# Kernel optimization log

Hardware: AMD Instinct MI355X
Metric: run time of the kernel (lower is better)

## Reference

```python
import jax, jax.numpy as jnp
import numpy as np

EPS = 1e-5

def conv2d(x, w, b=None, pad=0, groups=1):
    # x: NCHW, w: OIHW
    y = jax.lax.conv_general_dilated(
        x, w, window_strides=(1, 1), padding=[(pad, pad), (pad, pad)],
        dimension_numbers=('NCHW', 'OIHW', 'NCHW'), feature_group_count=groups)
    if b is not None:
        y = y + b[None, :, None, None]
    return y

def layernorm_c(x, w, b):
    # WithBias LayerNorm over channel dim of NCHW (matches to_3d -> LN(last dim=c) -> to_4d)
    mu = jnp.mean(x, axis=1, keepdims=True)
    var = jnp.mean((x - mu) ** 2, axis=1, keepdims=True)
    return (x - mu) / jnp.sqrt(var + EPS) * w[None, :, None, None] + b[None, :, None, None]

def setup_inputs() -> dict:
    key = jax.random.key(0)
    ks = iter(jax.random.split(key, 40))
    C, C8, Cc, Cs = 64, 8, 21, 2  # dim, dim//8, dim//compress_ratio, dim//squeeze_factor
    H = W = 64
    B = 4
    Hm = 128  # mlp hidden = dim * mlp_ratio
    s = 0.05
    def rn(shape):
        return jax.random.normal(next(ks), shape, dtype=jnp.float32) * s
    return {
        'x': jax.random.normal(next(ks), (B, C, H, W), dtype=jnp.float32),
        'ln_w': jnp.ones((C,), jnp.float32),
        'ln_b': jnp.zeros((C,), jnp.float32),
        'sab_q_w': rn((C8, C, 1, 1)), 'sab_q_b': rn((C8,)),
        'sab_k_w': rn((C8, C, 1, 1)), 'sab_k_b': rn((C8,)),
        'sab_v_w': rn((C, C, 1, 1)), 'sab_v_b': rn((C,)),
        'sab_qkdw_w': rn((C8, 1, 3, 3)), 'sab_qkdw_b': rn((C8,)),
        'sab_vdw_w': rn((C, 1, 3, 3)), 'sab_vdw_b': rn((C,)),
        'sab_proj_w': rn((C, C, 1, 1)), 'sab_proj_b': rn((C,)),
        'sab_gamma': jnp.zeros((1,), jnp.float32) + 0.1,
        'cab_w1': rn((Cc, C, 3, 3)), 'cab_b1': rn((Cc,)),
        'cab_w2': rn((C, Cc, 3, 3)), 'cab_b2': rn((C,)),
        'ca_w1': rn((Cs, C, 1, 1)), 'ca_b1': rn((Cs,)),
        'ca_w2': rn((C, Cs, 1, 1)), 'ca_b2': rn((C,)),
        'fc1_w': rn((Hm, C)), 'fc1_b': rn((Hm,)),
        'fc2_w': rn((C, Hm)), 'fc2_b': rn((C,)),
    }

def reference(x, ln_w, ln_b,
              sab_q_w, sab_q_b, sab_k_w, sab_k_b, sab_v_w, sab_v_b,
              sab_qkdw_w, sab_qkdw_b, sab_vdw_w, sab_vdw_b,
              sab_proj_w, sab_proj_b, sab_gamma,
              cab_w1, cab_b1, cab_w2, cab_b2,
              ca_w1, ca_b1, ca_w2, ca_b2,
              fc1_w, fc1_b, fc2_w, fc2_b):
    b, c, h, w = x.shape
    hw = h * w
    shortcut = x
    xn = layernorm_c(x, ln_w, ln_b)

    # --- SAB: full-pixel spatial self-attention ---
    C8 = sab_q_w.shape[0]
    q = conv2d(conv2d(xn, sab_q_w, sab_q_b), sab_qkdw_w, sab_qkdw_b, pad=1, groups=C8)
    k = conv2d(conv2d(xn, sab_k_w, sab_k_b), sab_qkdw_w, sab_qkdw_b, pad=1, groups=C8)
    v = conv2d(conv2d(xn, sab_v_w, sab_v_b), sab_vdw_w, sab_vdw_b, pad=1, groups=c)
    qf = q.reshape(b, C8, hw)          # (b, c8, n)
    kf = k.reshape(b, C8, hw)
    vf = v.reshape(b, c, hw)
    energy = jnp.einsum('bdi,bdj->bij', qf, kf)      # (b, hw, hw)
    attn = jax.nn.softmax(energy, axis=-1)
    out = jnp.einsum('bcj,bij->bci', vf, attn)        # (b, c, hw)
    out = out.reshape(b, c, h, w)
    out = conv2d(out, sab_proj_w, sab_proj_b)
    sa_feat = sab_gamma[0] * out + xn

    # --- CAB: conv compress/expand + RCAN channel attention ---
    y = conv2d(xn, cab_w1, cab_b1, pad=1)
    y = jax.nn.gelu(y, approximate=False)
    y = conv2d(y, cab_w2, cab_b2, pad=1)
    p = jnp.mean(y, axis=(2, 3), keepdims=True)       # adaptive avg pool to 1x1
    p = jax.nn.relu(conv2d(p, ca_w1, ca_b1))
    p = jax.nn.sigmoid(conv2d(p, ca_w2, ca_b2))
    ca_feat = y * p

    feat_sum = sa_feat + ca_feat + shortcut

    # --- MLP over channels (note: output is reshaped, NOT permuted back — faithful to source) ---
    fs1 = layernorm_c(feat_sum, ln_w, ln_b)
    t = fs1.transpose(0, 2, 3, 1).reshape(b, hw, c)   # (b, hw, c)
    t = jax.nn.gelu(t @ fc1_w.T + fc1_b, approximate=False)
    t = t @ fc2_w.T + fc2_b
    feat_sum2 = t.reshape(b, c, h, w)                 # raw view, matching torch .view(b,c,h,w)
    return feat_sum2 + feat_sum
```

## Files before the change

kernel.cpp:

```cpp
#include <hip/hip_runtime.h>
#include <math.h>

#define NB 4
#define NC 64
#define NC8 8
#define NCC 21
#define NHW 4096
#define NHM 128

typedef __attribute__((ext_vector_type(8))) short bf16x8;
typedef __attribute__((ext_vector_type(8))) unsigned short ushort8;
typedef __attribute__((ext_vector_type(4))) float f32x4;

__device__ __forceinline__ float gelu_exact(float x) {
    return 0.5f * x * (1.0f + erff(x * 0.70710678118654752f));
}

__device__ __forceinline__ unsigned short f2bf(float x) {
    union { float f; unsigned u; } u; u.f = x;
    unsigned r = u.u + 0x7fffu + ((u.u >> 16) & 1u);
    return (unsigned short)(r >> 16);
}

__device__ __forceinline__ float bf2f(unsigned short v) {
    union { unsigned u; float f; } t; t.u = (unsigned)v << 16; return t.f;
}

__global__ void k_wt(const float* __restrict__ qw, const float* __restrict__ kw,
                     const float* __restrict__ vw, const float* __restrict__ c1w,
                     const float* __restrict__ c2w, const float* __restrict__ pw,
                     const float* __restrict__ f1w, const float* __restrict__ f2w,
                     float* __restrict__ o, float* __restrict__ pool) {
    int idx = blockIdx.x * 256 + threadIdx.x;
    if (idx < 256) pool[idx] = 0.f;
    if (idx < 5120) {
        int ci = idx / 80, j = idx - ci * 80;
        float v = j < 8 ? qw[j * 64 + ci] : (j < 16 ? kw[(j - 8) * 64 + ci] : vw[(j - 16) * 64 + ci]);
        o[idx] = v;
    } else if (idx < 9216) {
        int r = idx - 5120; int co = r & 63, ci = r >> 6;
        o[idx] = pw[co * 64 + ci];
    } else if (idx < 17408) {
        int r = idx - 9216; int m = r & 127, c = r >> 7;
        o[idx] = f1w[m * 64 + c];
    } else if (idx < 25600) {
        int r = idx - 17408; int wo = r & 63, m = r >> 6;
        o[idx] = f2w[wo * 128 + m];
    } else if (idx < 44032) {
        int r = idx - 25600;
        int j = r & 7, l = (r >> 3) & 63, s = (r >> 9) % 18, f = r / 9216;
        int co = f * 16 + (l & 15);
        int k = s * 32 + (l >> 4) * 8 + j;
        int tap = k >> 6, ci = k & 63;
        float v = (co < 21) ? c1w[co * 576 + ci * 9 + tap] : 0.f;
        unsigned short hi = f2bf(v);
        unsigned short lo = f2bf(v - bf2f(hi));
        ((unsigned short*)(o + 25600))[r] = hi;
        ((unsigned short*)(o + 34816))[r] = lo;
    } else if (idx < 62464) {
        int r = idx - 44032;
        int j = r & 7, l = (r >> 3) & 63, s = (r >> 9) % 9, f = r / 4608;
        int co = f * 16 + (l & 15);
        int ci = (l >> 4) * 8 + j;
        float v = (ci < 21) ? c2w[co * 189 + ci * 9 + s] : 0.f;
        unsigned short hi = f2bf(v);
        unsigned short lo = f2bf(v - bf2f(hi));
        ((unsigned short*)(o + 44032))[r] = hi;
        ((unsigned short*)(o + 53248))[r] = lo;
    }
}

__global__ __launch_bounds__(256) void k_ln(const float* __restrict__ in, const float* __restrict__ w,
                                            const float* __restrict__ bb,
                                            unsigned short* __restrict__ out,
                                            unsigned short* __restrict__ outT) {
    __shared__ float r1[4][64], r2[4][64];
    int tid = threadIdx.x;
    int pl = tid & 63, cq = tid >> 6;
    int b = blockIdx.x >> 6;
    int pix = (blockIdx.x & 63) * 64 + pl;
    const float* p = in + (size_t)b * NC * NHW + pix;
    float v[16]; float s = 0.f, ss = 0.f;
    #pragma unroll
    for (int k = 0; k < 16; ++k) {
        float f = p[(size_t)(cq * 16 + k) * NHW];
        v[k] = f; s += f; ss += f * f;
    }
    r1[cq][pl] = s; r2[cq][pl] = ss;
    __syncthreads();
    float S  = r1[0][pl] + r1[1][pl] + r1[2][pl] + r1[3][pl];
    float SS = r2[0][pl] + r2[1][pl] + r2[2][pl] + r2[3][pl];
    float mean = S * (1.0f / 64);
    float rstd = rsqrtf(SS * (1.0f / 64) - mean * mean + 1e-5f);
    unsigned short* q = out + (size_t)b * NC * NHW + pix;
    ushort8 t0, t1;
    #pragma unroll
    for (int k = 0; k < 16; ++k) {
        int c = cq * 16 + k;
        unsigned short bv = f2bf((v[k] - mean) * rstd * w[c] + bb[c]);
        q[(size_t)c * NHW] = bv;
        if (k < 8) t0[k] = bv; else t1[k - 8] = bv;
    }
    unsigned short* tp = outT + ((size_t)b * NHW + pix) * 64 + cq * 16;
    *(ushort8*)tp = t0;
    *(ushort8*)(tp + 8) = t1;
}

__global__ __launch_bounds__(512) void k_qkv(const unsigned short* __restrict__ xn,
        const float* __restrict__ wt, const float* __restrict__ qb,
        const float* __restrict__ kb, const float* __restrict__ vb,
        unsigned short* __restrict__ q1, unsigned short* __restrict__ k1,
        unsigned short* __restrict__ v1) {
    __shared__ unsigned short Xs[64][64];
    __shared__ float Ws[64][80];
    int tid = threadIdx.x;
    int pix0 = blockIdx.x * 64, b = blockIdx.y;
    for (int i = tid; i < 1024; i += 512) {
        int c = i >> 4, q4 = i & 15;
        *(ushort4*)&Xs[c][q4 * 4] = *(const ushort4*)(xn + ((size_t)b * NC + c) * NHW + pix0 + q4 * 4);
    }
    for (int i = tid; i < 1280; i += 512)
        *(float4*)&((float*)Ws)[i * 4] = *(const float4*)&wt[i * 4];
    __syncthreads();
    int p2 = (tid & 31) * 2, g = tid >> 5;
    int co0 = g * 5;
    float a0[5], a1[5];
// ... 1 lines not shown
    for (int j = 0; j < 5; ++j) { a0[j] = 0.f; a1[j] = 0.f; }
    for (int ci = 0; ci < 64; ++ci) {
        ushort2 uv = *(const ushort2*)&Xs[ci][p2];
        float fx = bf2f(uv.x), fy = bf2f(uv.y);
        #pragma unroll
        for (int j = 0; j < 5; ++j) {
            float wv = Ws[ci][co0 + j];
            a0[j] = fmaf(fx, wv, a0[j]);
            a1[j] = fmaf(fy, wv, a1[j]);
        }
    }
    #pragma unroll
    for (int j = 0; j < 5; ++j) {
        int co = co0 + j;
        float bsv; unsigned short* dst;
        if (co < 8)       { bsv = qb[co];      dst = q1 + ((size_t)b * NC8 + co) * NHW + pix0 + p2; }
        else if (co < 16) { bsv = kb[co - 8];  dst = k1 + ((size_t)b * NC8 + co - 8) * NHW + pix0 + p2; }
        else              { bsv = vb[co - 16]; dst = v1 + ((size_t)b * NC + co - 16) * NHW + pix0 + p2; }
        ushort2 o = { f2bf(a0[j] + bsv), f2bf(a1[j] + bsv) };
        *(ushort2*)dst = o;
    }
}

__global__ void k_dw(const unsigned short* __restrict__ q1, const unsigned short* __restrict__ k1,
                     const unsigned short* __restrict__ v1,
                     const float* __restrict__ qkw, const float* __restrict__ qkb,
                     const float* __restrict__ vw, const float* __restrict__ vb,
                     unsigned short* __restrict__ qdb, unsigned short* __restrict__ kdb,
                     unsigned short* __restrict__ v8) {
    int pix = blockIdx.x * blockDim.x + threadIdx.x;
    int yv = blockIdx.y, b = blockIdx.z;
    int y = pix >> 6, x = pix & 63;
    if (yv < 16) {
        int c = yv & 7;
        const unsigned short* ip = (yv < 8 ? q1 : k1) + ((size_t)b * NC8 + c) * NHW;
        const float* wp = qkw + c * 9;
        float acc = qkb[c];
        #pragma unroll
        for (int dy = -1; dy <= 1; ++dy) {
            int yy = y + dy; if (yy < 0 || yy > 63) continue;
            #pragma unroll
            for (int dx = -1; dx <= 1; ++dx) {
                int xx = x + dx; if (xx < 0 || xx > 63) continue;
                acc += wp[(dy + 1) * 3 + (dx + 1)] * bf2f(ip[yy * 64 + xx]);
            }
        }
        (yv < 8 ? qdb : kdb)[((size_t)b * NHW + pix) * NC8 + c] = f2bf(acc);
    } else {
        int c = yv - 16;
        const unsigned short* ip = v1 + ((size_t)b * NC + c) * NHW;
        const float* wp = vw + c * 9;
        float acc = vb[c];
        #pragma unroll
        for (int dy = -1; dy <= 1; ++dy) {
            int yy = y + dy; if (yy < 0 || yy > 63) continue;
            #pragma unroll
            for (int dx = -1; dx <= 1; ++dx) {
                int xx = x + dx; if (xx < 0 || xx > 63) continue;
                acc += wp[(dy + 1) * 3 + (dx + 1)] * bf2f(ip[yy * 64 + xx]);
            }
        }
        v8[(((size_t)b * 512 + (pix >> 3)) * NC + c) * 8 + (pix & 7)] = f2bf(acc);
    }
}

__global__ __launch_bounds__(512) void k_cab1(const unsigned short* __restrict__ xnT,
        const unsigned short* __restrict__ Ah, const unsigned short* __restrict__ Al,
        const float* __restrict__ bias, unsigned short* __restrict__ y1T) {
    __shared__ float Rs[2048];
    int tid = threadIdx.x;
    int w = tid >> 6, lane = tid & 63;
    int il = lane & 15, g = lane >> 4;
    int frag = w & 3, kh = w >> 2;
    int y = blockIdx.x, b = blockIdx.y;
    int xloc = frag * 16 + il;
    f32x4 acc[2];
    acc[0] = (f32x4){0.f, 0.f, 0.f, 0.f};
    acc[1] = (f32x4){0.f, 0.f, 0.f, 0.f};
    #pragma unroll
    for (int si = 0; si < 9; ++si) {
        int s = kh * 9 + si;
        int tap = s >> 1;
        int ci0 = (s & 1) * 32;
        int dyv = tap / 3 - 1, dxv = tap - (tap / 3) * 3 - 1;
        int xx = xloc + dxv, yy = y + dyv;
        bf16x8 bv = (bf16x8)(short)0;
        if (((unsigned)xx < 64u) && ((unsigned)yy < 64u))
            bv = *(const bf16x8*)(xnT + ((size_t)b * NHW + yy * 64 + xx) * 64 + ci0 + g * 8);
        #pragma unroll
        for (int f = 0; f < 2; ++f) {
            bf16x8 ahv = *(const bf16x8*)(Ah + ((size_t)(f * 18 + s) * 64 + lane) * 8);
            bf16x8 alv = *(const bf16x8*)(Al + ((size_t)(f * 18 + s) * 64 + lane) * 8);
            acc[f] = __builtin_amdgcn_mfma_f32_16x16x32_bf16(ahv, bv, acc[f], 0, 0, 0);
            acc[f] = __builtin_amdgcn_mfma_f32_16x16x32_bf16(alv, bv, acc[f], 0, 0, 0);
        }
    }
    if (kh == 1) {
        #pragma unroll
        for (int f = 0; f < 2; ++f)
            #pragma unroll
            for (int e = 0; e < 4; ++e)
                Rs[((frag * 2 + f) * 4 + e) * 64 + lane] = acc[f][e];
    }
    __syncthreads();
    if (kh == 0) {
        #pragma unroll
        for (int f = 0; f < 2; ++f) {
            ushort4 pk;
            #pragma unroll
            for (int e = 0; e < 4; ++e) {
                float v = acc[f][e] + Rs[((frag * 2 + f) * 4 + e) * 64 + lane];
                int co = f * 16 + g * 4 + e;
                float r = 0.f;
                if (co < 21) r = gelu_exact(v + bias[co]);
                ((unsigned short*)&pk)[e] = f2bf(r);
            }
            *(ushort4*)(y1T + ((size_t)b * NHW + y * 64 + xloc) * 32 + f * 16 + g * 4) = pk;
        }
    }
}

__global__ __launch_bounds__(512) void k_cab2(const unsigned short* __restrict__ y1T,
        const unsigned short* __restrict__ Ah, const unsigned short* __restrict__ Al,
        const float* __restrict__ bias, unsigned short* __restrict__ ycT,
        float* __restrict__ pool) {
    __shared__ float Rs[4096];
    __shared__ float Ssum[4][64];
    int tid = threadIdx.x;
    int w = tid >> 6, lane = tid & 63;
    int il = lane & 15, g = lane >> 4;
    int frag = w & 3, kh = w >> 2;
    int y = blockIdx.x, b = blockIdx.y;
    int xloc = frag * 16 + il;
    f32x4 acc[4];
    #pragma unroll
    for (int f = 0; f < 4; ++f) acc[f] = (f32x4){0.f, 0.f, 0.f, 0.f};
    #pragma unroll
    for (int si = 0; si < 5; ++si) {
        if (!(kh == 1 && si == 4)) {
            int s = kh * 5 + si;
            int dyv = s / 3 - 1, dxv = s - (s / 3) * 3 - 1;
            int xx = xloc + dxv, yy = y + dyv;
            bf16x8 bv = (bf16x8)(short)0;
            if (((unsigned)xx < 64u) && ((unsigned)yy < 64u))
                bv = *(const bf16x8*)(y1T + ((size_t)b * NHW + yy * 64 + xx) * 32 + g * 8);
            #pragma unroll
            for (int f = 0; f < 4; ++f) {
                bf16x8 ahv = *(const bf16x8*)(Ah + ((size_t)(f * 9 + s) * 64 + lane) * 8);
                bf16x8 alv = *(const bf16x8*)(Al + ((size_t)(f * 9 + s) * 64 + lane) * 8);
                acc[f] = __builtin_amdgcn_mfma_f32_16x16x32_bf16(ahv, bv, acc[f], 0, 0, 0);
                acc[f] = __builtin_amdgcn_mfma_f32_16x16x32_bf16(alv, bv, acc[f], 0, 0, 0);
            }
        }
    }
    if (kh == 1) {
// ... 7 lines not shown
    if (kh == 0) {
        #pragma unroll
        for (int f = 0; f < 4; ++f) {
            ushort4 pk;
            #pragma unroll
            for (int e = 0; e < 4; ++e) {
                int co = f * 16 + g * 4 + e;
                float v = acc[f][e] + Rs[((frag * 4 + f) * 4 + e) * 64 + lane] + bias[co];
                ((unsigned short*)&pk)[e] = f2bf(v);
                float ps = v;
                ps += __shfl_xor(ps, 1, 64);
                ps += __shfl_xor(ps, 2, 64);
                ps += __shfl_xor(ps, 4, 64);
                ps += __shfl_xor(ps, 8, 64);
                if (il == 0) Ssum[frag][co] = ps;
            }
            *(ushort4*)(ycT + ((size_t)b * NHW + y * 64 + xloc) * 64 + f * 16 + g * 4) = pk;
        }
    }
    __syncthreads();
    if (tid < 64) {
        float t = Ssum[0][tid] + Ssum[1][tid] + Ssum[2][tid] + Ssum[3][tid];
        atomicAdd(&pool[b * NC + tid], t);
    }
}

__global__ __launch_bounds__(512) void k_flash(const unsigned short* __restrict__ qdb,
                                               const unsigned short* __restrict__ kdb,
                                               const unsigned short* __restrict__ v8,
                                               unsigned short* __restrict__ O) {
    __shared__ __align__(16) char smem[35840];
    int tid = threadIdx.x;
    int w = tid >> 6, lane = tid & 63;
    int g = lane >> 4, il = lane & 15;
    int i0 = blockIdx.x * 32, b = blockIdx.y;

    unsigned short (*P)[72] = (unsigned short (*)[72])(smem + w * 2304);

    bf16x8 qb0 = (bf16x8)(short)0, qb1 = (bf16x8)(short)0;
    if (g == 0) {
        qb0 = *(const bf16x8*)(qdb + (size_t)(b * NHW + i0 + il) * NC8);
        qb1 = *(const bf16x8*)(qdb + (size_t)(b * NHW + i0 + 16 + il) * NC8);
    }

    f32x4 acc0[4], acc1[4];
    #pragma unroll
    for (int ct = 0; ct < 4; ++ct) {
        acc0[ct] = (f32x4){0.f, 0.f, 0.f, 0.f};
        acc1[ct] = (f32x4){0.f, 0.f, 0.f, 0.f};
    }
    float La0 = 0.f, La1 = 0.f;

    bf16x8 kn[4];
    #pragma unroll
    for (int t = 0; t < 4; ++t) {
        kn[t] = (bf16x8)(short)0;
        if (g == 0) kn[t] = *(const bf16x8*)(kdb + (size_t)(b * NHW + w * 512 + 16 * t + il) * NC8);
    }

    for (int jt = 0; jt < 8; ++jt) {
        int j0 = w * 512 + jt * 64;
        int ch0 = b * 512 + (j0 >> 3);
        bf16x8 va[2][4];
        #pragma unroll
        for (int kc = 0; kc < 2; ++kc)
            #pragma unroll
            for (int ct = 0; ct < 4; ++ct)
                va[kc][ct] = *(const bf16x8*)(v8 +
                    ((size_t)(ch0 + kc * 4 + g) * NC + ct * 16 + il) * 8);
        bf16x8 ka[4];
        #pragma unroll
        for (int t = 0; t < 4; ++t) ka[t] = kn[t];
        if (jt < 7) {
            #pragma unroll
            for (int t = 0; t < 4; ++t) {
                kn[t] = (bf16x8)(short)0;
                if (g == 0) kn[t] = *(const bf16x8*)(kdb + (size_t)(b * NHW + j0 + 64 + 16 * t + il) * NC8);
            }
        }
        #pragma unroll
        for (int t = 0; t < 4; ++t) {
            f32x4 sv = __builtin_amdgcn_mfma_f32_16x16x32_bf16(ka[t], qb0, (f32x4){0.f, 0.f, 0.f, 0.f}, 0, 0, 0);
            float p0 = __expf(sv[0]), p1 = __expf(sv[1]);
            float p2 = __expf(sv[2]), p3 = __expf(sv[3]);
            La0 += (p0 + p1) + (p2 + p3);
            ushort4 pk;
            pk.x = f2bf(p0); pk.y = f2bf(p1); pk.z = f2bf(p2); pk.w = f2bf(p3);
            *(ushort4*)&P[il][16 * t + 4 * g] = pk;
        }
        #pragma unroll
        for (int kc = 0; kc < 2; ++kc) {
            bf16x8 pb = *(const bf16x8*)&P[il][kc * 32 + 8 * g];
            #pragma unroll
            for (int ct = 0; ct < 4; ++ct)
                acc0[ct] = __builtin_amdgcn_mfma_f32_16x16x32_bf16(va[kc][ct], pb, acc0[ct], 0, 0, 0);
        }
        #pragma unroll
        for (int t = 0; t < 4; ++t) {
            f32x4 sv = __builtin_amdgcn_mfma_f32_16x16x32_bf16(ka[t], qb1, (f32x4){0.f, 0.f, 0.f, 0.f}, 0, 0, 0);
            float p0 = __expf(sv[0]), p1 = __expf(sv[1]);
            float p2 = __expf(sv[2]), p3 = __expf(sv[3]);
            La1 += (p0 + p1) + (p2 + p3);
            ushort4 pk;
            pk.x = f2bf(p0); pk.y = f2bf(p1); pk.z = f2bf(p2); pk.w = f2bf(p3);
            *(ushort4*)&P[il][16 * t + 4 * g] = pk;
        }
        #pragma unroll
        for (int kc = 0; kc < 2; ++kc) {
            bf16x8 pb = *(const bf16x8*)&P[il][kc * 32 + 8 * g];
            #pragma unroll
            for (int ct = 0; ct < 4; ++ct)
                acc1[ct] = __builtin_amdgcn_mfma_f32_16x16x32_bf16(va[kc][ct], pb, acc1[ct], 0, 0, 0);
        }
    }
    La0 += __shfl_xor(La0, 16, 64); La0 += __shfl_xor(La0, 32, 64);
    La1 += __shfl_xor(La1, 16, 64); La1 += __shfl_xor(La1, 32, 64);

    __syncthreads();
    unsigned short* Ocm = (unsigned short*)smem;
    float* Lw = (float*)(smem + 34816);
    #pragma unroll
    for (int ct = 0; ct < 4; ++ct)
        #pragma unroll
        for (int e = 0; e < 4; ++e) {
            int c = ct * 16 + 4 * g + e;
            Ocm[(w * 2 + 0) * 1088 + c * 17 + il] = f2bf(acc0[ct][e]);
            Ocm[(w * 2 + 1) * 1088 + c * 17 + il] = f2bf(acc1[ct][e]);
        }
    if (lane < 16) {
        Lw[(w * 2 + 0) * 16 + il] = La0;
        Lw[(w * 2 + 1) * 16 + il] = La1;
    }
    __syncthreads();

    int st = tid >> 8, rem = tid & 255;
    int ic = rem & 15, ch = rem >> 4;
    float l = 0.f;
    #pragma unroll
    for (int w2 = 0; w2 < 8; ++w2) l += Lw[(w2 * 2 + st) * 16 + ic];
    float rl = 1.0f / l;
    #pragma unroll
    for (int cc = 0; cc < 4; ++cc) {
        int c = cc * 16 + ch;
        float o = 0.f;
        #pragma unroll
        for (int w2 = 0; w2 < 8; ++w2) o += bf2f(Ocm[(w2 * 2 + st) * 1088 + c * 17 + ic]);
        O[(size_t)(b * NC + c) * NHW + i0 + st * 16 + ic] = f2bf(o * rl);
    }
}

__global__ __launch_bounds__(512) void k_fsum2(const unsigned short* __restrict__ O,
        const float* __restrict__ pwt, const float* __restrict__ pb,
        const float* __restrict__ gamma, const unsigned short* __restrict__ xnT,
        const unsigned short* __restrict__ ycT, const float* __restrict__ pool,
        const float* __restrict__ cw1, const float* __restrict__ cb1,
        const float* __restrict__ cw2, const float* __restrict__ cb2,
        const float* __restrict__ x, const float* __restrict__ lnw,
        const float* __restrict__ lnb, unsigned short* __restrict__ fsum,
        unsigned short* __restrict__ fs1) {
    __shared__ unsigned short Os[64][64];
    __shared__ float Ws[64][64];
    __shared__ float Fs[64][66];
    __shared__ float mean_s[64], rstd_s[64];
    int tid = threadIdx.x;
    int pix0 = blockIdx.x * 64, b = blockIdx.y;
    for (int i = tid; i < 1024; i += 512) {
        int c = i >> 4, q4 = i & 15;
        *(ushort4*)&Os[c][q4 * 4] = *(const ushort4*)(O + ((size_t)b * NC + c) * NHW + pix0 + q4 * 4);
    }
    for (int i = tid; i < 1024; i += 512)
// ... 52 lines not shown
    }
    __syncthreads();
    if (tid < 64) {
        float s = 0.f, ss = 0.f;
        for (int c = 0; c < 64; ++c) { float v = Fs[c][tid]; s += v; ss += v * v; }
        float mean = s * (1.0f / 64);
        mean_s[tid] = mean;
        rstd_s[tid] = rsqrtf(ss * (1.0f / 64) - mean * mean + 1e-5f);
    }
    __syncthreads();
    float m0 = mean_s[p2], r0 = rstd_s[p2];
    float m1 = mean_s[p2 + 1], r1 = rstd_s[p2 + 1];
    #pragma unroll
    for (int j = 0; j < 4; ++j) {
        int c = co0 + j;
        size_t n = base + (size_t)c * NHW;
        float lw = lnw[c], lb = lnb[c];
        ushort2 o = { f2bf((f0[j] - m0) * r0 * lw + lb),
                      f2bf((f1[j] - m1) * r1 * lw + lb) };
        *(ushort2*)&fs1[n] = o;
    }
}

__global__ __launch_bounds__(512) void k_mlp1(const unsigned short* __restrict__ fs1,
        const float* __restrict__ wt, const float* __restrict__ bias,
        unsigned short* __restrict__ h) {
    __shared__ unsigned short Fs[64][64];
    __shared__ float Ws[64][128];
    int tid = threadIdx.x;
    int pix0 = blockIdx.x * 64, b = blockIdx.y;
    for (int i = tid; i < 1024; i += 512) {
        int c = i >> 4, q4 = i & 15;
        *(ushort4*)&Fs[c][q4 * 4] = *(const ushort4*)(fs1 + ((size_t)b * NC + c) * NHW + pix0 + q4 * 4);
    }
    for (int i = tid; i < 2048; i += 512)
        *(float4*)&((float*)Ws)[i * 4] = *(const float4*)&wt[i * 4];
    __syncthreads();
    int p2 = (tid & 31) * 2, g = tid >> 5;
    int m0 = g * 8;
    float a0[8], a1[8];
    #pragma unroll
    for (int j = 0; j < 8; ++j) { float bv = bias[m0 + j]; a0[j] = bv; a1[j] = bv; }
    for (int c = 0; c < 64; ++c) {
        ushort2 uv = *(const ushort2*)&Fs[c][p2];
        float vx = bf2f(uv.x), vy = bf2f(uv.y);
        float wv[8];
        *(float4*)&wv[0] = *(const float4*)&Ws[c][m0];
        *(float4*)&wv[4] = *(const float4*)&Ws[c][m0 + 4];
        #pragma unroll
        for (int j = 0; j < 8; ++j) {
            a0[j] = fmaf(vx, wv[j], a0[j]);
            a1[j] = fmaf(vy, wv[j], a1[j]);
        }
    }
    unsigned short* hp = h + (size_t)b * NHM * NHW + pix0 + p2;
    #pragma unroll
    for (int j = 0; j < 8; ++j) {
        ushort2 o = { f2bf(gelu_exact(a0[j])), f2bf(gelu_exact(a1[j])) };
        *(ushort2*)(hp + (size_t)(m0 + j) * NHW) = o;
    }
}

__global__ __launch_bounds__(512) void k_mlp2(const unsigned short* __restrict__ h,
        const float* __restrict__ wt, const float* __restrict__ bias,
        const unsigned short* __restrict__ fs, float* __restrict__ out) {
    __shared__ unsigned short Hs[128][64];
    __shared__ float Ws[128][64];
    int tid = threadIdx.x;
    int pix0 = blockIdx.x * 64, b = blockIdx.y;
    for (int i = tid; i < 2048; i += 512) {
        int m = i >> 4, q4 = i & 15;
        *(ushort4*)&Hs[m][q4 * 4] = *(const ushort4*)(h + ((size_t)b * NHM + m) * NHW + pix0 + q4 * 4);
    }
    for (int i = tid; i < 2048; i += 512)
        *(float4*)&((float*)Ws)[i * 4] = *(const float4*)&wt[i * 4];
    __syncthreads();
    int p2 = (tid & 31) * 2, g = tid >> 5;
    int wo0 = g * 4;
    float a0[4], a1[4];
    #pragma unroll
    for (int j = 0; j < 4; ++j) { float bv = bias[wo0 + j]; a0[j] = bv; a1[j] = bv; }
    for (int m = 0; m < 128; ++m) {
        ushort2 uv = *(const ushort2*)&Hs[m][p2];
        float vx = bf2f(uv.x), vy = bf2f(uv.y);
        float wv[4];
        *(float4*)wv = *(const float4*)&Ws[m][wo0];
        #pragma unroll
        for (int j = 0; j < 4; ++j) {
            a0[j] = fmaf(vx, wv[j], a0[j]);
            a1[j] = fmaf(vy, wv[j], a1[j]);
        }
    }
    size_t ob0 = ((size_t)b * NHW + pix0 + p2) * 64 + wo0;
    ushort4 r0 = *(const ushort4*)&fs[ob0];
    ushort4 r1 = *(const ushort4*)&fs[ob0 + 64];
    float4 w0, w1;
    w0.x = a0[0] + bf2f(r0.x); w0.y = a0[1] + bf2f(r0.y);
    w0.z = a0[2] + bf2f(r0.z); w0.w = a0[3] + bf2f(r0.w);
    w1.x = a1[0] + bf2f(r1.x); w1.y = a1[1] + bf2f(r1.y);
    w1.z = a1[2] + bf2f(r1.z); w1.w = a1[3] + bf2f(r1.w);
    *(float4*)&out[ob0] = w0;
    *(float4*)&out[ob0 + 64] = w1;
}

extern "C" void kernel_launch(void* const* d_in, const int* in_sizes, int n_in,
                              void* d_out, int out_size, void* d_ws, size_t ws_size,
                              hipStream_t stream) {
    const float* x        = (const float*)d_in[0];
    const float* ln_w     = (const float*)d_in[1];
// ... 22 lines not shown
    const float* fc1_w    = (const float*)d_in[24];
    const float* fc1_b    = (const float*)d_in[25];
    const float* fc2_w    = (const float*)d_in[26];
    const float* fc2_b    = (const float*)d_in[27];
    float* out = (float*)d_out;

    char* ws = (char*)d_ws;
    size_t off = 0;
    auto alloc = [&](size_t bytes) { void* p = ws + off; off += (bytes + 255) & ~(size_t)255; return p; };
    unsigned short* xn  = (unsigned short*)alloc((size_t)NB * NC * NHW * 2);
    unsigned short* xnT = (unsigned short*)alloc((size_t)NB * NHW * NC * 2);
    unsigned short* q1  = (unsigned short*)alloc((size_t)NB * NC8 * NHW * 2);
    unsigned short* k1  = (unsigned short*)alloc((size_t)NB * NC8 * NHW * 2);
    unsigned short* v1  = (unsigned short*)alloc((size_t)NB * NC * NHW * 2);
    unsigned short* qdb = (unsigned short*)alloc((size_t)NB * NHW * NC8 * 2);
    unsigned short* kdb = (unsigned short*)alloc((size_t)NB * NHW * NC8 * 2);
    unsigned short* vdb = (unsigned short*)alloc((size_t)NB * NC * NHW * 2);
    unsigned short* O   = (unsigned short*)alloc((size_t)NB * NC * NHW * 2);
    unsigned short* y1T = (unsigned short*)alloc((size_t)NB * NHW * 32 * 2);
    unsigned short* ycT = (unsigned short*)alloc((size_t)NB * NHW * NC * 2);
    float* pool  = (float*)alloc(256 * 4);
    unsigned short* fsum = (unsigned short*)alloc((size_t)NB * NC * NHW * 2);
    unsigned short* fs1  = (unsigned short*)alloc((size_t)NB * NC * NHW * 2);
    unsigned short* hbuf = (unsigned short*)alloc((size_t)NB * NHM * NHW * 2);
    float* wpack = (float*)alloc(62464 * 4);

    float* qkv_wt  = wpack;
    float* proj_wt = wpack + 5120;
    float* fc1_wt  = wpack + 9216;
    float* fc2_wt  = wpack + 17408;
    unsigned short* cab1Ah = (unsigned short*)(wpack + 25600);
    unsigned short* cab1Al = (unsigned short*)(wpack + 34816);
    unsigned short* cab2Ah = (unsigned short*)(wpack + 44032);
    unsigned short* cab2Al = (unsigned short*)(wpack + 53248);

    dim3 blk(256);
    dim3 blk5(512);

    k_wt<<<dim3(244), blk, 0, stream>>>(q_w, k_w, v_w, cab_w1, cab_w2, proj_w, fc1_w, fc2_w, wpack, pool);
    k_ln<<<dim3(256), blk, 0, stream>>>(x, ln_w, ln_b, xn, xnT);
    k_qkv<<<dim3(64, NB), blk5, 0, stream>>>(xn, qkv_wt, q_b, k_b, v_b, q1, k1, v1);
    k_dw<<<dim3(16, 80, NB), blk, 0, stream>>>(q1, k1, v1, qkdw_w, qkdw_b, vdw_w, vdw_b, qdb, kdb, vdb);
    k_cab1<<<dim3(64, NB), blk5, 0, stream>>>(xnT, cab1Ah, cab1Al, cab_b1, y1T);
    k_flash<<<dim3(128, NB), blk5, 0, stream>>>(qdb, kdb, vdb, O);
    k_cab2<<<dim3(64, NB), blk5, 0, stream>>>(y1T, cab2Ah, cab2Al, cab_b2, ycT, pool);
    k_fsum2<<<dim3(64, NB), blk5, 0, stream>>>(O, proj_wt, proj_b, gamma, xnT, ycT, pool,
                                               ca_w1, ca_b1, ca_w2, ca_b2, x, ln_w, ln_b,
                                               fsum, fs1);
    k_mlp1<<<dim3(64, NB), blk5, 0, stream>>>(fs1, fc1_wt, fc1_b, hbuf);
    k_mlp2<<<dim3(64, NB), blk5, 0, stream>>>(hbuf, fc2_wt, fc2_b, fsum, out);
}
```

Measured before the change: 206.8 us.

## Merge independent kernels into shared launches and fuse MLP stages in shared memory

```diff
diff --git a/kernel.cpp b/kernel.cpp
--- a/kernel.cpp
+++ b/kernel.cpp
@@ -26,60 +26,62 @@
     union { unsigned u; float f; } t; t.u = (unsigned)v << 16; return t.f;
 }
 
-__global__ void k_wt(const float* __restrict__ qw, const float* __restrict__ kw,
+__global__ __launch_bounds__(256) void k_prep(const float* __restrict__ qw, const float* __restrict__ kw,
                      const float* __restrict__ vw, const float* __restrict__ c1w,
                      const float* __restrict__ c2w, const float* __restrict__ pw,
                      const float* __restrict__ f1w, const float* __restrict__ f2w,
-                     float* __restrict__ o, float* __restrict__ pool) {
-    int idx = blockIdx.x * 256 + threadIdx.x;
-    if (idx < 256) pool[idx] = 0.f;
-    if (idx < 5120) {
-        int ci = idx / 80, j = idx - ci * 80;
-        float v = j < 8 ? qw[j * 64 + ci] : (j < 16 ? kw[(j - 8) * 64 + ci] : vw[(j - 16) * 64 + ci]);
-        o[idx] = v;
-    } else if (idx < 9216) {
-        int r = idx - 5120; int co = r & 63, ci = r >> 6;
-        o[idx] = pw[co * 64 + ci];
-    } else if (idx < 17408) {
-        int r = idx - 9216; int m = r & 127, c = r >> 7;
-        o[idx] = f1w[m * 64 + c];
-    } else if (idx < 25600) {
-        int r = idx - 17408; int wo = r & 63, m = r >> 6;
-        o[idx] = f2w[wo * 128 + m];
-    } else if (idx < 44032) {
-        int r = idx - 25600;
-        int j = r & 7, l = (r >> 3) & 63, s = (r >> 9) % 18, f = r / 9216;
-        int co = f * 16 + (l & 15);
-        int k = s * 32 + (l >> 4) * 8 + j;
-        int tap = k >> 6, ci = k & 63;
-        float v = (co < 21) ? c1w[co * 576 + ci * 9 + tap] : 0.f;
-        unsigned short hi = f2bf(v);
-        unsigned short lo = f2bf(v - bf2f(hi));
-        ((unsigned short*)(o + 25600))[r] = hi;
-        ((unsigned short*)(o + 34816))[r] = lo;
-    } else if (idx < 62464) {
-        int r = idx - 44032;
-        int j = r & 7, l = (r >> 3) & 63, s = (r >> 9) % 9, f = r / 4608;
-        int co = f * 16 + (l & 15);
-        int ci = (l >> 4) * 8 + j;
-        float v = (ci < 21) ? c2w[co * 189 + ci * 9 + s] : 0.f;
-        unsigned short hi = f2bf(v);
-        unsigned short lo = f2bf(v - bf2f(hi));
-        ((unsigned short*)(o + 44032))[r] = hi;
-        ((unsigned short*)(o + 53248))[r] = lo;
-    }
-}
-
-__global__ __launch_bounds__(256) void k_ln(const float* __restrict__ in, const float* __restrict__ w,
-                                            const float* __restrict__ bb,
-                                            unsigned short* __restrict__ out,
-                                            unsigned short* __restrict__ outT) {
+                     float* __restrict__ o, float* __restrict__ pool,
+                     const float* __restrict__ x, const float* __restrict__ lnw,
+                     const float* __restrict__ lnb,
+                     unsigned short* __restrict__ xn, unsigned short* __restrict__ xnT) {
+    int bid = blockIdx.x;
+    int tid = threadIdx.x;
+    if (bid < 244) {
+        int idx = bid * 256 + tid;
+        if (idx < 256) pool[idx] = 0.f;
+        if (idx < 5120) {
+            int ci = idx / 80, j = idx - ci * 80;
+            float v = j < 8 ? qw[j * 64 + ci] : (j < 16 ? kw[(j - 8) * 64 + ci] : vw[(j - 16) * 64 + ci]);
+            o[idx] = v;
+        } else if (idx < 9216) {
+            int r = idx - 5120; int co = r & 63, ci = r >> 6;
+            o[idx] = pw[co * 64 + ci];
+        } else if (idx < 17408) {
+            int r = idx - 9216; int m = r & 127, c = r >> 7;
+            o[idx] = f1w[m * 64 + c];
+        } else if (idx < 25600) {
+            int r = idx - 17408; int wo = r & 63, m = r >> 6;
+            o[idx] = f2w[wo * 128 + m];
+        } else if (idx < 44032) {
+            int r = idx - 25600;
+            int j = r & 7, l = (r >> 3) & 63, s = (r >> 9) % 18, f = r / 9216;
+            int co = f * 16 + (l & 15);
+            int k = s * 32 + (l >> 4) * 8 + j;
+            int tap = k >> 6, ci = k & 63;
+            float v = (co < 21) ? c1w[co * 576 + ci * 9 + tap] : 0.f;
+            unsigned short hi = f2bf(v);
+            unsigned short lo = f2bf(v - bf2f(hi));
+            ((unsigned short*)(o + 25600))[r] = hi;
+            ((unsigned short*)(o + 34816))[r] = lo;
+        } else if (idx < 62464) {
+            int r = idx - 44032;
+            int j = r & 7, l = (r >> 3) & 63, s = (r >> 9) % 9, f = r / 4608;
+            int co = f * 16 + (l & 15);
+            int ci = (l >> 4) * 8 + j;
+            float v = (ci < 21) ? c2w[co * 189 + ci * 9 + s] : 0.f;
+            unsigned short hi = f2bf(v);
+            unsigned short lo = f2bf(v - bf2f(hi));
+            ((unsigned short*)(o + 44032))[r] = hi;
+            ((unsigned short*)(o + 53248))[r] = lo;
+        }
+        return;
+    }
     __shared__ float r1[4][64], r2[4][64];
-    int tid = threadIdx.x;
+    int lb = bid - 244;
     int pl = tid & 63, cq = tid >> 6;
-    int b = blockIdx.x >> 6;
-    int pix = (blockIdx.x & 63) * 64 + pl;
-    const float* p = in + (size_t)b * NC * NHW + pix;
+    int b = lb >> 6;
+    int pix = (lb & 63) * 64 + pl;
+    const float* p = x + (size_t)b * NC * NHW + pix;
     float v[16]; float s = 0.f, ss = 0.f;
     #pragma unroll
     for (int k = 0; k < 16; ++k) {
@@ -92,16 +94,16 @@
     float SS = r2[0][pl] + r2[1][pl] + r2[2][pl] + r2[3][pl];
     float mean = S * (1.0f / 64);
     float rstd = rsqrtf(SS * (1.0f / 64) - mean * mean + 1e-5f);
-    unsigned short* q = out + (size_t)b * NC * NHW + pix;
+    unsigned short* q = xn + (size_t)b * NC * NHW + pix;
     ushort8 t0, t1;
     #pragma unroll
     for (int k = 0; k < 16; ++k) {
         int c = cq * 16 + k;
-        unsigned short bv = f2bf((v[k] - mean) * rstd * w[c] + bb[c]);
+        unsigned short bv = f2bf((v[k] - mean) * rstd * lnw[c] + lnb[c]);
         q[(size_t)c * NHW] = bv;
         if (k < 8) t0[k] = bv; else t1[k - 8] = bv;
     }
-    unsigned short* tp = outT + ((size_t)b * NHW + pix) * 64 + cq * 16;
+    unsigned short* tp = xnT + ((size_t)b * NHW + pix) * 64 + cq * 16;
     *(ushort8*)tp = t0;
     *(ushort8*)(tp + 8) = t1;
 }
@@ -149,57 +151,62 @@
     }
 }
 
-__global__ void k_dw(const unsigned short* __restrict__ q1, const unsigned short* __restrict__ k1,
-                     const unsigned short* __restrict__ v1,
-                     const float* __restrict__ qkw, const float* __restrict__ qkb,
-                     const float* __restrict__ vw, const float* __restrict__ vb,
-                     unsigned short* __restrict__ qdb, unsigned short* __restrict__ kdb,
-                     unsigned short* __restrict__ v8) {
-    int pix = blockIdx.x * blockDim.x + threadIdx.x;
-    int yv = blockIdx.y, b = blockIdx.z;
-    int y = pix >> 6, x = pix & 63;
-    if (yv < 16) {
-        int c = yv & 7;
-        const unsigned short* ip = (yv < 8 ? q1 : k1) + ((size_t)b * NC8 + c) * NHW;
-        const float* wp = qkw + c * 9;
-        float acc = qkb[c];
-        #pragma unroll
-        for (int dy = -1; dy <= 1; ++dy) {
-            int yy = y + dy; if (yy < 0 || yy > 63) continue;
-            #pragma unroll
-            for (int dx = -1; dx <= 1; ++dx) {
-                int xx = x + dx; if (xx < 0 || xx > 63) continue;
-                acc += wp[(dy + 1) * 3 + (dx + 1)] * bf2f(ip[yy * 64 + xx]);
-            }
-        }
-        (yv < 8 ? qdb : kdb)[((size_t)b * NHW + pix) * NC8 + c] = f2bf(acc);
-    } else {
-        int c = yv - 16;
-        const unsigned short* ip = v1 + ((size_t)b * NC + c) * NHW;
-        const float* wp = vw + c * 9;
-        float acc = vb[c];
-        #pragma unroll
-        for (int dy = -1; dy <= 1; ++dy) {
-            int yy = y + dy; if (yy < 0 || yy > 63) continue;
-            #pragma unroll
-            for (int dx = -1; dx <= 1; ++dx) {
-                int xx = x + dx; if (xx < 0 || xx > 63) continue;
-                acc += wp[(dy + 1) * 3 + (dx + 1)] * bf2f(ip[yy * 64 + xx]);
-            }
-        }
-        v8[(((size_t)b * 512 + (pix >> 3)) * NC + c) * 8 + (pix & 7)] = f2bf(acc);
-    }
-}
-
-__global__ __launch_bounds__(512) void k_cab1(const unsigned short* __restrict__ xnT,
+__global__ __launch_bounds__(512) void k_dwcab1(
+        const unsigned short* __restrict__ q1, const unsigned short* __restrict__ k1,
+        const unsigned short* __restrict__ v1,
+        const float* __restrict__ qkw, const float* __restrict__ qkb,
+        const float* __restrict__ vw, const float* __restrict__ vb,
+        unsigned short* __restrict__ qdb, unsigned short* __restrict__ kdb,
+        unsigned short* __restrict__ v8,
+        const unsigned short* __restrict__ xnT,
         const unsigned short* __restrict__ Ah, const unsigned short* __restrict__ Al,
         const float* __restrict__ bias, unsigned short* __restrict__ y1T) {
     __shared__ float Rs[2048];
+    int bid = blockIdx.x;
     int tid = threadIdx.x;
+    if (bid < 2560) {
+        int pix = (bid & 7) * 512 + tid;
+        int rest = bid >> 3;
+        int yv = rest % 80, b = rest / 80;
+        int y = pix >> 6, x = pix & 63;
+        if (yv < 16) {
+            int c = yv & 7;
+            const unsigned short* ip = (yv < 8 ? q1 : k1) + ((size_t)b * NC8 + c) * NHW;
+            const float* wp = qkw + c * 9;
+            float acc = qkb[c];
+            #pragma unroll
+            for (int dy = -1; dy <= 1; ++dy) {
+                int yy = y + dy; if (yy < 0 || yy > 63) continue;
+                #pragma unroll
+                for (int dx = -1; dx <= 1; ++dx) {
+                    int xx = x + dx; if (xx < 0 || xx > 63) continue;
+                    acc += wp[(dy + 1) * 3 + (dx + 1)] * bf2f(ip[yy * 64 + xx]);
+                }
+            }
+            (yv < 8 ? qdb : kdb)[((size_t)b * NHW + pix) * NC8 + c] = f2bf(acc);
+        } else {
+            int c = yv - 16;
+            const unsigned short* ip = v1 + ((size_t)b * NC + c) * NHW;
+            const float* wp = vw + c * 9;
+            float acc = vb[c];
+            #pragma unroll
+            for (int dy = -1; dy <= 1; ++dy) {
+                int yy = y + dy; if (yy < 0 || yy > 63) continue;
+                #pragma unroll
+                for (int dx = -1; dx <= 1; ++dx) {
+                    int xx = x + dx; if (xx < 0 || xx > 63) continue;
+                    acc += wp[(dy + 1) * 3 + (dx + 1)] * bf2f(ip[yy * 64 + xx]);
+                }
+            }
+            v8[(((size_t)b * 512 + (pix >> 3)) * NC + c) * 8 + (pix & 7)] = f2bf(acc);
+        }
+        return;
+    }
+    int r = bid - 2560;
+    int y = r & 63, b = r >> 6;
     int w = tid >> 6, lane = tid & 63;
     int il = lane & 15, g = lane >> 4;
     int frag = w & 3, kh = w >> 2;
-    int y = blockIdx.x, b = blockIdx.y;
     int xloc = frag * 16 + il;
     f32x4 acc[2];
     acc[0] = (f32x4){0.f, 0.f, 0.f, 0.f};
@@ -238,26 +245,144 @@
             for (int e = 0; e < 4; ++e) {
                 float v = acc[f][e] + Rs[((frag * 2 + f) * 4 + e) * 64 + lane];
                 int co = f * 16 + g * 4 + e;
-                float r = 0.f;
-                if (co < 21) r = gelu_exact(v + bias[co]);
-                ((unsigned short*)&pk)[e] = f2bf(r);
+                float rr = 0.f;
+                if (co < 21) rr = gelu_exact(v + bias[co]);
+                ((unsigned short*)&pk)[e] = f2bf(rr);
             }
             *(ushort4*)(y1T + ((size_t)b * NHW + y * 64 + xloc) * 32 + f * 16 + g * 4) = pk;
         }
     }
 }
 
-__global__ __launch_bounds__(512) void k_cab2(const unsigned short* __restrict__ y1T,
+__global__ __launch_bounds__(512) void k_flashcab2(
+        const unsigned short* __restrict__ qdb, const unsigned short* __restrict__ kdb,
+        const unsigned short* __restrict__ v8, unsigned short* __restrict__ O,
+        const unsigned short* __restrict__ y1T,
         const unsigned short* __restrict__ Ah, const unsigned short* __restrict__ Al,
         const float* __restrict__ bias, unsigned short* __restrict__ ycT,
         float* __restrict__ pool) {
-    __shared__ float Rs[4096];
-    __shared__ float Ssum[4][64];
+    __shared__ __align__(16) char smem[35840];
+    int bid = blockIdx.x;
     int tid = threadIdx.x;
     int w = tid >> 6, lane = tid & 63;
-    int il = lane & 15, g = lane >> 4;
+    int g = lane >> 4, il = lane & 15;
+    if (bid < 512) {
+        int i0 = (bid & 127) * 32, b = bid >> 7;
+        unsigned short (*P)[72] = (unsigned short (*)[72])(smem + w * 2304);
+        bf16x8 qb0 = (bf16x8)(short)0, qb1 = (bf16x8)(short)0;
+        if (g == 0) {
+            qb0 = *(const bf16x8*)(qdb + (size_t)(b * NHW + i0 + il) * NC8);
+            qb1 = *(const bf16x8*)(qdb + (size_t)(b * NHW + i0 + 16 + il) * NC8);
+        }
+        f32x4 acc0[4], acc1[4];
+        #pragma unroll
+        for (int ct = 0; ct < 4; ++ct) {
+            acc0[ct] = (f32x4){0.f, 0.f, 0.f, 0.f};
+            acc1[ct] = (f32x4){0.f, 0.f, 0.f, 0.f};
+        }
+        float La0 = 0.f, La1 = 0.f;
+        bf16x8 kn[4];
+        #pragma unroll
+        for (int t = 0; t < 4; ++t) {
+            kn[t] = (bf16x8)(short)0;
+            if (g == 0) kn[t] = *(const bf16x8*)(kdb + (size_t)(b * NHW + w * 512 + 16 * t + il) * NC8);
+        }
+        for (int jt = 0; jt < 8; ++jt) {
+            int j0 = w * 512 + jt * 64;
+            int ch0 = b * 512 + (j0 >> 3);
+            bf16x8 va[2][4];
+            #pragma unroll
+            for (int kc = 0; kc < 2; ++kc)
+                #pragma unroll
+                for (int ct = 0; ct < 4; ++ct)
+                    va[kc][ct] = *(const bf16x8*)(v8 +
+                        ((size_t)(ch0 + kc * 4 + g) * NC + ct * 16 + il) * 8);
+            bf16x8 ka[4];
+            #pragma unroll
+            for (int t = 0; t < 4; ++t) ka[t] = kn[t];
+            if (jt < 7) {
+                #pragma unroll
+                for (int t = 0; t < 4; ++t) {
+                    kn[t] = (bf16x8)(short)0;
+                    if (g == 0) kn[t] = *(const bf16x8*)(kdb + (size_t)(b * NHW + j0 + 64 + 16 * t + il) * NC8);
+                }
+            }
+            #pragma unroll
+            for (int t = 0; t < 4; ++t) {
+                f32x4 sv = __builtin_amdgcn_mfma_f32_16x16x32_bf16(ka[t], qb0, (f32x4){0.f, 0.f, 0.f, 0.f}, 0, 0, 0);
+                float p0 = __expf(sv[0]), p1 = __expf(sv[1]);
+                float p2 = __expf(sv[2]), p3 = __expf(sv[3]);
+                La0 += (p0 + p1) + (p2 + p3);
+                ushort4 pk;
+                pk.x = f2bf(p0); pk.y = f2bf(p1); pk.z = f2bf(p2); pk.w = f2bf(p3);
+                *(ushort4*)&P[il][16 * t + 4 * g] = pk;
+            }
+            #pragma unroll
+            for (int kc = 0; kc < 2; ++kc) {
+                bf16x8 pb = *(const bf16x8*)&P[il][kc * 32 + 8 * g];
+                #pragma unroll
+                for (int ct = 0; ct < 4; ++ct)
+                    acc0[ct] = __builtin_amdgcn_mfma_f32_16x16x32_bf16(va[kc][ct], pb, acc0[ct], 0, 0, 0);
+            }
+            #pragma unroll
+            for (int t = 0; t < 4; ++t) {
+                f32x4 sv = __builtin_amdgcn_mfma_f32_16x16x32_bf16(ka[t], qb1, (f32x4){0.f, 0.f, 0.f, 0.f}, 0, 0, 0);
+                float p0 = __expf(sv[0]), p1 = __expf(sv[1]);
+                float p2 = __expf(sv[2]), p3 = __expf(sv[3]);
+                La1 += (p0 + p1) + (p2 + p3);
+                ushort4 pk;
+                pk.x = f2bf(p0); pk.y = f2bf(p1); pk.z = f2bf(p2); pk.w = f2bf(p3);
+                *(ushort4*)&P[il][16 * t + 4 * g] = pk;
+            }
+            #pragma unroll
+            for (int kc = 0; kc < 2; ++kc) {
+                bf16x8 pb = *(const bf16x8*)&P[il][kc * 32 + 8 * g];
+                #pragma unroll
+                for (int ct = 0; ct < 4; ++ct)
+                    acc1[ct] = __builtin_amdgcn_mfma_f32_16x16x32_bf16(va[kc][ct], pb, acc1[ct], 0, 0, 0);
+            }
+        }
+        La0 += __shfl_xor(La0, 16, 64); La0 += __shfl_xor(La0, 32, 64);
+        La1 += __shfl_xor(La1, 16, 64); La1 += __shfl_xor(La1, 32, 64);
+
+        __syncthreads();
+        unsigned short* Ocm = (unsigned short*)smem;
+        float* Lw = (float*)(smem + 34816);
+        #pragma unroll
+        for (int ct = 0; ct < 4; ++ct)
+            #pragma unroll
+            for (int e = 0; e < 4; ++e) {
+                int c = ct * 16 + 4 * g + e;
+                Ocm[(w * 2 + 0) * 1088 + c * 17 + il] = f2bf(acc0[ct][e]);
+                Ocm[(w * 2 + 1) * 1088 + c * 17 + il] = f2bf(acc1[ct][e]);
+            }
+        if (lane < 16) {
+            Lw[(w * 2 + 0) * 16 + il] = La0;
+            Lw[(w * 2 + 1) * 16 + il] = La1;
+        }
+        __syncthreads();
+
+        int st = tid >> 8, rem = tid & 255;
+        int ic = rem & 15, ch = rem >> 4;
+        float l = 0.f;
+        #pragma unroll
+        for (int w2 = 0; w2 < 8; ++w2) l += Lw[(w2 * 2 + st) * 16 + ic];
+        float rl = 1.0f / l;
+        #pragma unroll
+        for (int cc = 0; cc < 4; ++cc) {
+            int c = cc * 16 + ch;
+            float o = 0.f;
+            #pragma unroll
+            for (int w2 = 0; w2 < 8; ++w2) o += bf2f(Ocm[(w2 * 2 + st) * 1088 + c * 17 + ic]);
+            O[(size_t)(b * NC + c) * NHW + i0 + st * 16 + ic] = f2bf(o * rl);
+        }
+        return;
+    }
+    float* Rs = (float*)smem;
+    float (*Ssum)[64] = (float (*)[64])(smem + 16384);
+    int r = bid - 512;
+    int y = r & 63, b = r >> 6;
     int frag = w & 3, kh = w >> 2;
-    int y = blockIdx.x, b = blockIdx.y;
     int xloc = frag * 16 + il;
     f32x4 acc[4];
     #pragma unroll
@@ -311,130 +436,6 @@
     if (tid < 64) {
         float t = Ssum[0][tid] + Ssum[1][tid] + Ssum[2][tid] + Ssum[3][tid];
         atomicAdd(&pool[b * NC + tid], t);
-    }
-}
-
-__global__ __launch_bounds__(512) void k_flash(const unsigned short* __restrict__ qdb,
-                                               const unsigned short* __restrict__ kdb,
-                                               const unsigned short* __restrict__ v8,
-                                               unsigned short* __restrict__ O) {
-    __shared__ __align__(16) char smem[35840];
-    int tid = threadIdx.x;
-    int w = tid >> 6, lane = tid & 63;
-    int g = lane >> 4, il = lane & 15;
-    int i0 = blockIdx.x * 32, b = blockIdx.y;
-
-    unsigned short (*P)[72] = (unsigned short (*)[72])(smem + w * 2304);
-
-    bf16x8 qb0 = (bf16x8)(short)0, qb1 = (bf16x8)(short)0;
-    if (g == 0) {
-        qb0 = *(const bf16x8*)(qdb + (size_t)(b * NHW + i0 + il) * NC8);
-        qb1 = *(const bf16x8*)(qdb + (size_t)(b * NHW + i0 + 16 + il) * NC8);
-    }
-
-    f32x4 acc0[4], acc1[4];
-    #pragma unroll
-    for (int ct = 0; ct < 4; ++ct) {
-        acc0[ct] = (f32x4){0.f, 0.f, 0.f, 0.f};
-        acc1[ct] = (f32x4){0.f, 0.f, 0.f, 0.f};
-    }
-    float La0 = 0.f, La1 = 0.f;
-
-    bf16x8 kn[4];
-    #pragma unroll
-    for (int t = 0; t < 4; ++t) {
-        kn[t] = (bf16x8)(short)0;
-        if (g == 0) kn[t] = *(const bf16x8*)(kdb + (size_t)(b * NHW + w * 512 + 16 * t + il) * NC8);
-    }
-
-    for (int jt = 0; jt < 8; ++jt) {
-        int j0 = w * 512 + jt * 64;
-        int ch0 = b * 512 + (j0 >> 3);
-        bf16x8 va[2][4];
-        #pragma unroll
-        for (int kc = 0; kc < 2; ++kc)
-            #pragma unroll
-            for (int ct = 0; ct < 4; ++ct)
-                va[kc][ct] = *(const bf16x8*)(v8 +
-                    ((size_t)(ch0 + kc * 4 + g) * NC + ct * 16 + il) * 8);
-        bf16x8 ka[4];
-        #pragma unroll
-        for (int t = 0; t < 4; ++t) ka[t] = kn[t];
-        if (jt < 7) {
-            #pragma unroll
-            for (int t = 0; t < 4; ++t) {
-                kn[t] = (bf16x8)(short)0;
-                if (g == 0) kn[t] = *(const bf16x8*)(kdb + (size_t)(b * NHW + j0 + 64 + 16 * t + il) * NC8);
-            }
-        }
-        #pragma unroll
-        for (int t = 0; t < 4; ++t) {
-            f32x4 sv = __builtin_amdgcn_mfma_f32_16x16x32_bf16(ka[t], qb0, (f32x4){0.f, 0.f, 0.f, 0.f}, 0, 0, 0);
-            float p0 = __expf(sv[0]), p1 = __expf(sv[1]);
-            float p2 = __expf(sv[2]), p3 = __expf(sv[3]);
-            La0 += (p0 + p1) + (p2 + p3);
-            ushort4 pk;
-            pk.x = f2bf(p0); pk.y = f2bf(p1); pk.z = f2bf(p2); pk.w = f2bf(p3);
-            *(ushort4*)&P[il][16 * t + 4 * g] = pk;
-        }
-        #pragma unroll
-        for (int kc = 0; kc < 2; ++kc) {
-            bf16x8 pb = *(const bf16x8*)&P[il][kc * 32 + 8 * g];
-            #pragma unroll
-            for (int ct = 0; ct < 4; ++ct)
-                acc0[ct] = __builtin_amdgcn_mfma_f32_16x16x32_bf16(va[kc][ct], pb, acc0[ct], 0, 0, 0);
-        }
-        #pragma unroll
-        for (int t = 0; t < 4; ++t) {
-            f32x4 sv = __builtin_amdgcn_mfma_f32_16x16x32_bf16(ka[t], qb1, (f32x4){0.f, 0.f, 0.f, 0.f}, 0, 0, 0);
-            float p0 = __expf(sv[0]), p1 = __expf(sv[1]);
-            float p2 = __expf(sv[2]), p3 = __expf(sv[3]);
-            La1 += (p0 + p1) + (p2 + p3);
-            ushort4 pk;
-            pk.x = f2bf(p0); pk.y = f2bf(p1); pk.z = f2bf(p2); pk.w = f2bf(p3);
-            *(ushort4*)&P[il][16 * t + 4 * g] = pk;
-        }
-        #pragma unroll
-        for (int kc = 0; kc < 2; ++kc) {
-            bf16x8 pb = *(const bf16x8*)&P[il][kc * 32 + 8 * g];
-            #pragma unroll
-            for (int ct = 0; ct < 4; ++ct)
-                acc1[ct] = __builtin_amdgcn_mfma_f32_16x16x32_bf16(va[kc][ct], pb, acc1[ct], 0, 0, 0);
-        }
-    }
-    La0 += __shfl_xor(La0, 16, 64); La0 += __shfl_xor(La0, 32, 64);
-    La1 += __shfl_xor(La1, 16, 64); La1 += __shfl_xor(La1, 32, 64);
-
-    __syncthreads();
-    unsigned short* Ocm = (unsigned short*)smem;
-    float* Lw = (float*)(smem + 34816);
-    #pragma unroll
-    for (int ct = 0; ct < 4; ++ct)
-        #pragma unroll
-        for (int e = 0; e < 4; ++e) {
-            int c = ct * 16 + 4 * g + e;
-            Ocm[(w * 2 + 0) * 1088 + c * 17 + il] = f2bf(acc0[ct][e]);
-            Ocm[(w * 2 + 1) * 1088 + c * 17 + il] = f2bf(acc1[ct][e]);
-        }
-    if (lane < 16) {
-        Lw[(w * 2 + 0) * 16 + il] = La0;
-        Lw[(w * 2 + 1) * 16 + il] = La1;
-    }
-    __syncthreads();
-
-    int st = tid >> 8, rem = tid & 255;
-    int ic = rem & 15, ch = rem >> 4;
-    float l = 0.f;
-    #pragma unroll
-    for (int w2 = 0; w2 < 8; ++w2) l += Lw[(w2 * 2 + st) * 16 + ic];
-    float rl = 1.0f / l;
-    #pragma unroll
-    for (int cc = 0; cc < 4; ++cc) {
-        int c = cc * 16 + ch;
-        float o = 0.f;
-        #pragma unroll
-        for (int w2 = 0; w2 < 8; ++w2) o += bf2f(Ocm[(w2 * 2 + st) * 1088 + c * 17 + ic]);
-        O[(size_t)(b * NC + c) * NHW + i0 + st * 16 + ic] = f2bf(o * rl);
     }
 }
 
@@ -533,11 +534,14 @@
     }
 }
 
-__global__ __launch_bounds__(512) void k_mlp1(const unsigned short* __restrict__ fs1,
-        const float* __restrict__ wt, const float* __restrict__ bias,
-        unsigned short* __restrict__ h) {
+__global__ __launch_bounds__(512) void k_mlp(const unsigned short* __restrict__ fs1,
+        const float* __restrict__ w1t, const float* __restrict__ b1,
+        const float* __restrict__ w2t, const float* __restrict__ b2,
+        const unsigned short* __restrict__ fs, float* __restrict__ out) {
     __shared__ unsigned short Fs[64][64];
-    __shared__ float Ws[64][128];
+    __shared__ float W1[64][128];
+    __shared__ unsigned short Hs[128][64];
+    __shared__ float W2[128][64];
     int tid = threadIdx.x;
     int pix0 = blockIdx.x * 64, b = blockIdx.y;
     for (int i = tid; i < 1024; i += 512) {
@@ -545,57 +549,44 @@
         *(ushort4*)&Fs[c][q4 * 4] = *(const ushort4*)(fs1 + ((size_t)b * NC + c) * NHW + pix0 + q4 * 4);
     }
     for (int i = tid; i < 2048; i += 512)
-        *(float4*)&((float*)Ws)[i * 4] = *(const float4*)&wt[i * 4];
+        *(float4*)&((float*)W1)[i * 4] = *(const float4*)&w1t[i * 4];
+    for (int i = tid; i < 2048; i += 512)
+        *(float4*)&((float*)W2)[i * 4] = *(const float4*)&w2t[i * 4];
     __syncthreads();
     int p2 = (tid & 31) * 2, g = tid >> 5;
-    int m0 = g * 8;
-    float a0[8], a1[8];
-    #pragma unroll
-    for (int j = 0; j < 8; ++j) { float bv = bias[m0 + j]; a0[j] = bv; a1[j] = bv; }
-    for (int c = 0; c < 64; ++c) {
-        ushort2 uv = *(const ushort2*)&Fs[c][p2];
-        float vx = bf2f(uv.x), vy = bf2f(uv.y);
-        float wv[8];
-        *(float4*)&wv[0] = *(const float4*)&Ws[c][m0];
-        *(float4*)&wv[4] = *(const float4*)&Ws[c][m0 + 4];
+    {
+        int m0 = g * 8;
+        float a0[8], a1[8];
+        #pragma unroll
+        for (int j = 0; j < 8; ++j) { float bv = b1[m0 + j]; a0[j] = bv; a1[j] = bv; }
+        for (int c = 0; c < 64; ++c) {
+            ushort2 uv = *(const ushort2*)&Fs[c][p2];
+            float vx = bf2f(uv.x), vy = bf2f(uv.y);
+            float wv[8];
+            *(float4*)&wv[0] = *(const float4*)&W1[c][m0];
+            *(float4*)&wv[4] = *(const float4*)&W1[c][m0 + 4];
+            #pragma unroll
+            for (int j = 0; j < 8; ++j) {
+                a0[j] = fmaf(vx, wv[j], a0[j]);
+                a1[j] = fmaf(vy, wv[j], a1[j]);
+            }
+        }
         #pragma unroll
         for (int j = 0; j < 8; ++j) {
-            a0[j] = fmaf(vx, wv[j], a0[j]);
-            a1[j] = fmaf(vy, wv[j], a1[j]);
-        }
-    }
-    unsigned short* hp = h + (size_t)b * NHM * NHW + pix0 + p2;
-    #pragma unroll
-    for (int j = 0; j < 8; ++j) {
-        ushort2 o = { f2bf(gelu_exact(a0[j])), f2bf(gelu_exact(a1[j])) };
-        *(ushort2*)(hp + (size_t)(m0 + j) * NHW) = o;
-    }
-}
-
-__global__ __launch_bounds__(512) void k_mlp2(const unsigned short* __restrict__ h,
-        const float* __restrict__ wt, const float* __restrict__ bias,
-        const unsigned short* __restrict__ fs, float* __restrict__ out) {
-    __shared__ unsigned short Hs[128][64];
-    __shared__ float Ws[128][64];
-    int tid = threadIdx.x;
-    int pix0 = blockIdx.x * 64, b = blockIdx.y;
-    for (int i = tid; i < 2048; i += 512) {
-        int m = i >> 4, q4 = i & 15;
-        *(ushort4*)&Hs[m][q4 * 4] = *(const ushort4*)(h + ((size_t)b * NHM + m) * NHW + pix0 + q4 * 4);
-    }
-    for (int i = tid; i < 2048; i += 512)
-        *(float4*)&((float*)Ws)[i * 4] = *(const float4*)&wt[i * 4];
-    __syncthreads();
-    int p2 = (tid & 31) * 2, g = tid >> 5;
+            ushort2 o = { f2bf(gelu_exact(a0[j])), f2bf(gelu_exact(a1[j])) };
+            *(ushort2*)&Hs[m0 + j][p2] = o;
+        }
+    }
+    __syncthreads();
     int wo0 = g * 4;
     float a0[4], a1[4];
     #pragma unroll
-    for (int j = 0; j < 4; ++j) { float bv = bias[wo0 + j]; a0[j] = bv; a1[j] = bv; }
+    for (int j = 0; j < 4; ++j) { float bv = b2[wo0 + j]; a0[j] = bv; a1[j] = bv; }
     for (int m = 0; m < 128; ++m) {
         ushort2 uv = *(const ushort2*)&Hs[m][p2];
         float vx = bf2f(uv.x), vy = bf2f(uv.y);
         float wv[4];
-        *(float4*)wv = *(const float4*)&Ws[m][wo0];
+        *(float4*)wv = *(const float4*)&W2[m][wo0];
         #pragma unroll
         for (int j = 0; j < 4; ++j) {
             a0[j] = fmaf(vx, wv[j], a0[j]);
@@ -664,7 +655,6 @@
     float* pool  = (float*)alloc(256 * 4);
     unsigned short* fsum = (unsigned short*)alloc((size_t)NB * NC * NHW * 2);
     unsigned short* fs1  = (unsigned short*)alloc((size_t)NB * NC * NHW * 2);
-    unsigned short* hbuf = (unsigned short*)alloc((size_t)NB * NHM * NHW * 2);
     float* wpack = (float*)alloc(62464 * 4);
 
     float* qkv_wt  = wpack;
@@ -679,16 +669,15 @@
     dim3 blk(256);
     dim3 blk5(512);
 
-    k_wt<<<dim3(244), blk, 0, stream>>>(q_w, k_w, v_w, cab_w1, cab_w2, proj_w, fc1_w, fc2_w, wpack, pool);
-    k_ln<<<dim3(256), blk, 0, stream>>>(x, ln_w, ln_b, xn, xnT);
+    k_prep<<<dim3(500), blk, 0, stream>>>(q_w, k_w, v_w, cab_w1, cab_w2, proj_w, fc1_w, fc2_w,
+                                          wpack, pool, x, ln_w, ln_b, xn, xnT);
     k_qkv<<<dim3(64, NB), blk5, 0, stream>>>(xn, qkv_wt, q_b, k_b, v_b, q1, k1, v1);
-    k_dw<<<dim3(16, 80, NB), blk, 0, stream>>>(q1, k1, v1, qkdw_w, qkdw_b, vdw_w, vdw_b, qdb, kdb, vdb);
-    k_cab1<<<dim3(64, NB), blk5, 0, stream>>>(xnT, cab1Ah, cab1Al, cab_b1, y1T);
-    k_flash<<<dim3(128, NB), blk5, 0, stream>>>(qdb, kdb, vdb, O);
-    k_cab2<<<dim3(64, NB), blk5, 0, stream>>>(y1T, cab2Ah, cab2Al, cab_b2, ycT, pool);
+    k_dwcab1<<<dim3(2816), blk5, 0, stream>>>(q1, k1, v1, qkdw_w, qkdw_b, vdw_w, vdw_b,
+                                              qdb, kdb, vdb, xnT, cab1Ah, cab1Al, cab_b1, y1T);
+    k_flashcab2<<<dim3(768), blk5, 0, stream>>>(qdb, kdb, vdb, O, y1T, cab2Ah, cab2Al,
+                                                cab_b2, ycT, pool);
     k_fsum2<<<dim3(64, NB), blk5, 0, stream>>>(O, proj_wt, proj_b, gamma, xnT, ycT, pool,
                                                ca_w1, ca_b1, ca_w2, ca_b2, x, ln_w, ln_b,
                                                fsum, fs1);
-    k_mlp1<<<dim3(64, NB), blk5, 0, stream>>>(fs1, fc1_wt, fc1_b, hbuf);
-    k_mlp2<<<dim3(64, NB), blk5, 0, stream>>>(hbuf, fc2_wt, fc2_b, fsum, out);
-}
+    k_mlp<<<dim3(64, NB), blk5, 0, stream>>>(fs1, fc1_wt, fc1_b, fc2_wt, fc2_b, fsum, out);
+}
```

Result: faster. 201.8 us (-2.4%).
